# Kernel tuning notes

Hardware: AMD Instinct MI355X
Metric: run time of the kernel (lower is better)

## Reference

```python
import jax, jax.numpy as jnp
import numpy as np

C = 128          # hidden_channels
N = 100000       # num nodes
E = 500000       # num edges
BN_EPS = 1e-5    # BatchNorm eps (training mode: batch statistics)


def _bn_relu(x, g, b):
    # BatchNorm1d (training mode, biased variance) followed by ReLU
    mu = x.mean(axis=0)
    var = x.var(axis=0)
    return jax.nn.relu(g * (x - mu) * jax.lax.rsqrt(var + BN_EPS) + b)


def setup_inputs() -> dict:
    key = jax.random.key(0)
    ks = jax.random.split(key, 10)
    f = lambda k, s: jax.random.normal(k, s, dtype=jnp.float32) * 0.05
    return {
        "node_rep": f(ks[0], (N, C)),
        "edge_rep": f(ks[1], (E, C)),
        "endpoints": jax.random.randint(ks[2], (2, E), 0, N, dtype=jnp.int64)
            if jax.config.jax_enable_x64 else jax.random.randint(ks[2], (2, E), 0, N, dtype=jnp.int32),
        # lvl_mlp_1: Linear(2C -> C, no bias) + BN(C)
        "W_lvl1": f(ks[3], (2 * C, C)),
        "g_lvl1": jnp.ones((C,), jnp.float32), "b_lvl1": jnp.zeros((C,), jnp.float32),
        # lvl_mlp_2: Linear(C->2C) + BN(2C) + ReLU + Linear(2C->C) + BN(C) + ReLU
        "W_n1": f(ks[4], (C, 2 * C)),
        "g_n1": jnp.ones((2 * C,), jnp.float32), "b_n1": jnp.zeros((2 * C,), jnp.float32),
        "W_n2": f(ks[5], (2 * C, C)),
        "g_n2": jnp.ones((C,), jnp.float32), "b_n2": jnp.zeros((C,), jnp.float32),
        # lift_mlp: Linear(C->2C) + BN(2C) + ReLU + Linear(2C->C) + BN(C) + ReLU
        "W_e1": f(ks[6], (C, 2 * C)),
        "g_e1": jnp.ones((2 * C,), jnp.float32), "b_e1": jnp.zeros((2 * C,), jnp.float32),
        "W_e2": f(ks[7], (2 * C, C)),
        "g_e2": jnp.ones((C,), jnp.float32), "b_e2": jnp.zeros((C,), jnp.float32),
        "eps1": jnp.zeros((), jnp.float32),
        "eps2": jnp.zeros((), jnp.float32),
    }


def reference(node_rep, edge_rep, endpoints,
              W_lvl1, g_lvl1, b_lvl1,
              W_n1, g_n1, b_n1, W_n2, g_n2, b_n2,
              W_e1, g_e1, b_e1, W_e2, g_e2, b_e2,
              eps1, eps2):
    s, t = endpoints[0], endpoints[1]
    # transfer0_0 node->edge: each edge sums its two endpoint node features
    lift_aggr = node_rep[s] + node_rep[t]                       # [E, C]
    h = _bn_relu(jnp.concatenate([lift_aggr, edge_rep], -1) @ W_lvl1,
                 g_lvl1, b_lvl1)                                # [E, C]
    # reverse transfer edge->node: scatter-add to both endpoints
    lvl_aggr = jnp.zeros_like(node_rep).at[s].add(h).at[t].add(h)  # [N, C]
    node_in = (1.0 + eps1) * node_rep + lvl_aggr
    node_out = _bn_relu(_bn_relu(node_in @ W_n1, g_n1, b_n1) @ W_n2, g_n2, b_n2)
    edge_in = (1.0 + eps2) * edge_rep + lift_aggr
    edge_out = _bn_relu(_bn_relu(edge_in @ W_e1, g_e1, b_e1) @ W_e2, g_e2, b_e2)
    return (node_out, edge_out)
```

## Files before the change

kernel.cpp:

```cpp
#include <hip/hip_runtime.h>

#define NN 100000
#define NE 500000

typedef short v8s __attribute__((ext_vector_type(8)));
typedef float v4f __attribute__((ext_vector_type(4)));

__device__ __forceinline__ unsigned short f2bf(float f) {
    unsigned u = __float_as_uint(f);
    u += 0x7fffu + ((u >> 16) & 1u);
    return (unsigned short)(u >> 16);
}
__device__ __forceinline__ float bf2f(unsigned short h) {
    return __uint_as_float(((unsigned)h) << 16);
}
__device__ __forceinline__ unsigned pk2(float a, float b) {
    return (unsigned)f2bf(a) | ((unsigned)f2bf(b) << 16);
}
__device__ __forceinline__ float lo16(unsigned v) { return bf2f((unsigned short)(v & 0xffffu)); }
__device__ __forceinline__ float hi16(unsigned v) { return bf2f((unsigned short)(v >> 16)); }

__global__ void detect_k(const unsigned short* __restrict__ edgeR, int* __restrict__ flag) {
    __shared__ int cnt;
    const int tid = threadIdx.x;
    if (tid == 0) cnt = 0;
    __syncthreads();
    const float v = fabsf(bf2f(edgeR[2 * tid]));
    const int sane = (v > 1e-5f && v < 100.f) ? 1 : 0;
    atomicAdd(&cnt, sane);
    __syncthreads();
    if (tid == 0) *flag = (cnt >= 128) ? 1 : 0;
}

__global__ __launch_bounds__(256) void convert_k(const void* __restrict__ src,
    unsigned short* __restrict__ dst, const long n4, const int* __restrict__ flag)
{
    const long i = (long)blockIdx.x * 256 + threadIdx.x;
    if (i >= n4) return;
    if (*flag) {
        ((uint2*)dst)[i] = ((const uint2*)src)[i];
    } else {
        const float4 f = ((const float4*)src)[i];
        uint2 o; o.x = pk2(f.x, f.y); o.y = pk2(f.z, f.w);
        ((uint2*)dst)[i] = o;
    }
}

__global__ __launch_bounds__(256) void pack_weights(
    const void* __restrict__ W1, const void* __restrict__ Wn1,
    const void* __restrict__ Wn2, const void* __restrict__ We1,
    const void* __restrict__ We2, unsigned short* __restrict__ wpk,
    const int* __restrict__ flag)
{
    const int i = blockIdx.x * 256 + threadIdx.x;
    if (i >= 163840) return;
    const void* W; int Nn; int li = i;
    if (i < 32768)       { W = W1;  Nn = 128; }
    else if (i < 65536)  { W = Wn1; Nn = 256; li -= 32768; }
    else if (i < 98304)  { W = Wn2; Nn = 128; li -= 65536; }
    else if (i < 131072) { W = We1; Nn = 256; li -= 98304; }
    else                 { W = We2; Nn = 128; li -= 131072; }
    const int ntn = Nn >> 4;
    const int j = li & 7, l = (li >> 3) & 63, tile = li >> 9;
    const int ct = tile % ntn, kt = tile / ntn;
    const int k = kt * 32 + (l >> 4) * 8 + j;
    const int n = ct * 16 + (l & 15);
    const int idx = k * Nn + n;
    wpk[i] = (*flag) ? ((const unsigned short*)W)[idx]
                     : f2bf(((const float*)W)[idx]);
}

__global__ __launch_bounds__(256) void kernel_A(
    const unsigned short* __restrict__ node, const unsigned short* __restrict__ edge,
    const int* __restrict__ ep,
    const unsigned short* __restrict__ wpk1, const unsigned short* __restrict__ wpkE1,
    unsigned short* __restrict__ y1, unsigned short* __restrict__ w1,
    float* __restrict__ stats, const void* __restrict__ eps2p, const int* __restrict__ flag)
{
    __shared__ unsigned short X[64][264];
    const int tid = threadIdx.x, wid = tid >> 6, lane = tid & 63;
    const int mrow = lane & 15, quad = lane >> 4;
    const long e0 = (long)blockIdx.x * 64;
    const int bin = blockIdx.x & 7;

    for (int rr = 0; rr < 16; ++rr) {
        const int r = wid * 16 + rr;
        const long e = e0 + r;
        unsigned lp = 0, epk = 0;
        if (e < NE) {
            const int s = ep[e], t = ep[NE + e];
            const unsigned a = ((const unsigned*)(node + (size_t)s * 128))[lane];
            const unsigned b = ((const unsigned*)(node + (size_t)t * 128))[lane];
            epk = ((const unsigned*)(edge + (size_t)e * 128))[lane];
            lp = pk2(lo16(a) + lo16(b), hi16(a) + hi16(b));
        }
        *(unsigned*)&X[r][2 * lane] = lp;
        *(unsigned*)&X[r][128 + 2 * lane] = epk;
    }
    __syncthreads();

    {
        v4f acc[4][2];
        #pragma unroll
        for (int rb = 0; rb < 4; ++rb)
            #pragma unroll
            for (int c = 0; c < 2; ++c)
                acc[rb][c] = (v4f){0.f, 0.f, 0.f, 0.f};
        const int ct0 = wid * 2;
        #pragma unroll
        for (int kt = 0; kt < 8; ++kt) {
            v8s a[4];
            #pragma unroll
            for (int rb = 0; rb < 4; ++rb)
                a[rb] = *(const v8s*)&X[rb * 16 + mrow][kt * 32 + quad * 8];
            #pragma unroll
            for (int c = 0; c < 2; ++c) {
                const v8s b = ((const v8s*)wpk1)[(kt * 8 + ct0 + c) * 64 + lane];
                #pragma unroll
                for (int rb = 0; rb < 4; ++rb)
                    acc[rb][c] = __builtin_amdgcn_mfma_f32_16x16x32_bf16(a[rb], b, acc[rb][c], 0, 0, 0);
            }
        }
        #pragma unroll
        for (int c = 0; c < 2; ++c) {
            const int col = (ct0 + c) * 16 + mrow;
            float sy = 0.f, sq = 0.f;
            #pragma unroll
            for (int rb = 0; rb < 4; ++rb) {
                #pragma unroll
                for (int r4 = 0; r4 < 4; ++r4) {
                    const float v = acc[rb][c][r4];
                    const long e = e0 + rb * 16 + quad * 4 + r4;
                    if (e < NE) y1[e * 128 + col] = f2bf(v);
                    sy += v; sq += v * v;
                }
            }
            sy += __shfl_xor(sy, 16); sy += __shfl_xor(sy, 32);
            sq += __shfl_xor(sq, 16); sq += __shfl_xor(sq, 32);
            if (quad == 0) {
                atomicAdd(&stats[bin * 1792 + col], sy);
                atomicAdd(&stats[bin * 1792 + 128 + col], sq);
            }
        }
    }
    __syncthreads();

    const float e2 = 1.f + ((*flag) ? bf2f(((const unsigned short*)eps2p)[0])
                                    : ((const float*)eps2p)[0]);
    for (int rr = 0; rr < 16; ++rr) {
        const int r = wid * 16 + rr;
        const unsigned lp = *(const unsigned*)&X[r][2 * lane];
        const unsigned ee = *(const unsigned*)&X[r][128 + 2 * lane];
        *(unsigned*)&X[r][2 * lane] = pk2(fmaf(e2, lo16(ee), lo16(lp)),
                                          fmaf(e2, hi16(ee), hi16(lp)));
    }
    __syncthreads();

    {
        v4f acc[4][4];
        #pragma unroll
        for (int rb = 0; rb < 4; ++rb)
            #pragma unroll
            for (int c = 0; c < 4; ++c)
                acc[rb][c] = (v4f){0.f, 0.f, 0.f, 0.f};
        const int ct0 = wid * 4;
        #pragma unroll
        for (int kt = 0; kt < 4; ++kt) {
            v8s a[4];
            #pragma unroll
            for (int rb = 0; rb < 4; ++rb)
                a[rb] = *(const v8s*)&X[rb * 16 + mrow][kt * 32 + quad * 8];
            #pragma unroll
            for (int c = 0; c < 4; ++c) {
                const v8s b = ((const v8s*)wpkE1)[(kt * 16 + ct0 + c) * 64 + lane];
                #pragma unroll
                for (int rb = 0; rb < 4; ++rb)
                    acc[rb][c] = __builtin_amdgcn_mfma_f32_16x16x32_bf16(a[rb], b, acc[rb][c], 0, 0, 0);
            }
        }
        #pragma unroll
        for (int c = 0; c < 4; ++c) {
            const int col = (ct0 + c) * 16 + mrow;
            float sy = 0.f, sq = 0.f;
            #pragma unroll
            for (int rb = 0; rb < 4; ++rb) {
                #pragma unroll
                for (int r4 = 0; r4 < 4; ++r4) {
                    const float v = acc[rb][c][r4];
                    const long e = e0 + rb * 16 + quad * 4 + r4;
                    if (e < NE) w1[e * 256 + col] = f2bf(v);
                    sy += v; sq += v * v;
                }
            }
            sy += __shfl_xor(sy, 16); sy += __shfl_xor(sy, 32);
            sq += __shfl_xor(sq, 16); sq += __shfl_xor(sq, 32);
            if (quad == 0) {
                atomicAdd(&stats[bin * 1792 + 256 + col], sy);
                atomicAdd(&stats[bin * 1792 + 512 + col], sq);
            }
        }
    }
}

__global__ void finalize_k(const float* __restrict__ stats, float* __restrict__ ab,
                           const void* __restrict__ g, const void* __restrict__ bb,
                           const int sOff, const int qOff, const int aOff, const int bOff,
                           const int n, const float invc, const int* __restrict__ flag)
{
    const int c = threadIdx.x;
    if (c >= n) return;
    float S = 0.f, Q = 0.f;
    for (int b = 0; b < 8; ++b) { S += stats[b * 1792 + sOff + c]; Q += stats[b * 1792 + qOff + c]; }
    const float mu = S * invc;
    const float var = Q * invc - mu * mu;
    const float gv = (*flag) ? bf2f(((const unsigned short*)g)[c]) : ((const float*)g)[c];
    const float bv = (*flag) ? bf2f(((const unsigned short*)bb)[c]) : ((const float*)bb)[c];
    const float a = gv * rsqrtf(var + 1e-5f);
    ab[aOff + c] = a;
    ab[bOff + c] = bv - a * mu;
}

__global__ __launch_bounds__(256) void scatter_k(
    const unsigned short* __restrict__ y1, const int* __restrict__ ep,
    const float* __restrict__ ab, float* __restrict__ acc)
{
    const int gw = (blockIdx.x * 256 + threadIdx.x) >> 6;
    const int lane = threadIdx.x & 63;
    const int nw = (gridDim.x * 256) >> 6;
    const int c0 = 2 * lane;
    const float a0 = ab[c0], a1 = ab[c0 + 1];
    const float b0 = ab[128 + c0], b1 = ab[128 + c0 + 1];
    for (long e = gw; e < NE; e += nw) {
        const unsigned v = *(const unsigned*)(y1 + e * 128 + c0);
        const float h0 = fmaxf(fmaf(a0, lo16(v), b0), 0.f);
        const float h1 = fmaxf(fmaf(a1, hi16(v), b1), 0.f);
        const int s = ep[e], t = ep[NE + e];
        atomicAdd(&acc[(size_t)s * 128 + c0], h0);
        atomicAdd(&acc[(size_t)s * 128 + c0 + 1], h1);
        atomicAdd(&acc[(size_t)t * 128 + c0], h0);
        atomicAdd(&acc[(size_t)t * 128 + c0 + 1], h1);
    }
}

__global__ __launch_bounds__(256) void gemm_node1(
    const unsigned short* __restrict__ node, const float* __restrict__ aggr,
    const unsigned short* __restrict__ wpk, unsigned short* __restrict__ z1,
    float* __restrict__ sS, float* __restrict__ sQ,
    const void* __restrict__ eps1p, const int* __restrict__ flag)
{
    __shared__ unsigned short X[64][136];
    const int tid = threadIdx.x, wid = tid >> 6, lane = tid & 63;
    const int mrow = lane & 15, quad = lane >> 4;
    const long r0 = (long)blockIdx.x * 64;
    const int bin = blockIdx.x & 7;
    const float ea = 1.f + ((*flag) ? bf2f(((const unsigned short*)eps1p)[0])
                                    : ((const float*)eps1p)[0]);
    for (int rr = 0; rr < 16; ++rr) {
        const int r = wid * 16 + rr;
        const long gr = r0 + r;
        unsigned o = 0;
        if (gr < NN) {
            const unsigned nr = ((const unsigned*)(node + (size_t)gr * 128))[lane];
            const float2 ag = ((const float2*)(aggr + (size_t)gr * 128))[lane];
            o = pk2(fmaf(ea, lo16(nr), ag.x), fmaf(ea, hi16(nr), ag.y));
        }
        *(unsigned*)&X[r][2 * lane] = o;
    }
    __syncthreads();
    v4f acc[4][4];
    #pragma unroll
    for (int rb = 0; rb < 4; ++rb)
        #pragma unroll
        for (int c = 0; c < 4; ++c)
            acc[rb][c] = (v4f){0.f, 0.f, 0.f, 0.f};
    const int ct0 = wid * 4;
    #pragma unroll
    for (int kt = 0; kt < 4; ++kt) {
        v8s a[4];
        #pragma unroll
        for (int rb = 0; rb < 4; ++rb)
            a[rb] = *(const v8s*)&X[rb * 16 + mrow][kt * 32 + quad * 8];
        #pragma unroll
        for (int c = 0; c < 4; ++c) {
            const v8s b = ((const v8s*)wpk)[(kt * 16 + ct0 + c) * 64 + lane];
            #pragma unroll
            for (int rb = 0; rb < 4; ++rb)
                acc[rb][c] = __builtin_amdgcn_mfma_f32_16x16x32_bf16(a[rb], b, acc[rb][c], 0, 0, 0);
        }
    }
    #pragma unroll
    for (int c = 0; c < 4; ++c) {
        const int col = (ct0 + c) * 16 + mrow;
        float sy = 0.f, sq = 0.f;
        #pragma unroll
        for (int rb = 0; rb < 4; ++rb) {
            #pragma unroll
            for (int r4 = 0; r4 < 4; ++r4) {
                const float v = acc[rb][c][r4];
                const long gr = r0 + rb * 16 + quad * 4 + r4;
                if (gr < NN) z1[gr * 256 + col] = f2bf(v);
                sy += v; sq += v * v;
            }
        }
        sy += __shfl_xor(sy, 16); sy += __shfl_xor(sy, 32);
        sq += __shfl_xor(sq, 16); sq += __shfl_xor(sq, 32);
        if (quad == 0) {
            atomicAdd(&sS[bin * 1792 + col], sy);
            atomicAdd(&sQ[bin * 1792 + col], sq);
        }
    }
}

__global__ __launch_bounds__(256) void gemm_k256(
    const unsigned short* __restrict__ in, const float* __restrict__ aab,
    const float* __restrict__ bab, const unsigned short* __restrict__ wpk,
    unsigned short* __restrict__ out, float* __restrict__ sS, float* __restrict__ sQ,
    const long rows)
{
    __shared__ unsigned short X[64][264];
    const int tid = threadIdx.x, wid = tid >> 6, lane = tid & 63;
    const int mrow = lane & 15, quad = lane >> 4;
    const long r0 = (long)blockIdx.x * 64;
    const int bin = blockIdx.x & 7;
    const float4 av = ((const float4*)aab)[lane];
    const float4 bv = ((const float4*)bab)[lane];
    for (int rr = 0; rr < 16; ++rr) {
        const int r = wid * 16 + rr;
        const long gr = r0 + r;
        ushort4 o = {0, 0, 0, 0};
        if (gr < rows) {
            const ushort4 w = *(const ushort4*)(in + gr * 256 + 4 * lane);
            o.x = f2bf(fmaxf(fmaf(av.x, bf2f(w.x), bv.x), 0.f));
            o.y = f2bf(fmaxf(fmaf(av.y, bf2f(w.y), bv.y), 0.f));
            o.z = f2bf(fmaxf(fmaf(av.z, bf2f(w.z), bv.z), 0.f));
            o.w = f2bf(fmaxf(fmaf(av.w, bf2f(w.w), bv.w), 0.f));
        }
        *(ushort4*)&X[r][4 * lane] = o;
    }
    __syncthreads();
    v4f acc[4][2];
    #pragma unroll
    for (int rb = 0; rb < 4; ++rb)
        #pragma unroll
        for (int c = 0; c < 2; ++c)
            acc[rb][c] = (v4f){0.f, 0.f, 0.f, 0.f};
    const int ct0 = wid * 2;
    #pragma unroll
    for (int kt = 0; kt < 8; ++kt) {
        v8s a[4];
        #pragma unroll
        for (int rb = 0; rb < 4; ++rb)
            a[rb] = *(const v8s*)&X[rb * 16 + mrow][kt * 32 + quad * 8];
        #pragma unroll
        for (int c = 0; c < 2; ++c) {
            const v8s b = ((const v8s*)wpk)[(kt * 8 + ct0 + c) * 64 + lane];
            #pragma unroll
            for (int rb = 0; rb < 4; ++rb)
                acc[rb][c] = __builtin_amdgcn_mfma_f32_16x16x32_bf16(a[rb], b, acc[rb][c], 0, 0, 0);
        }
    }
    #pragma unroll
    for (int c = 0; c < 2; ++c) {
        const int col = (ct0 + c) * 16 + mrow;
        float sy = 0.f, sq = 0.f;
        #pragma unroll
        for (int rb = 0; rb < 4; ++rb) {
            #pragma unroll
            for (int r4 = 0; r4 < 4; ++r4) {
                const float v = acc[rb][c][r4];
                const long gr = r0 + rb * 16 + quad * 4 + r4;
                if (gr < rows) out[gr * 128 + col] = f2bf(v);
                sy += v; sq += v * v;
            }
        }
        sy += __shfl_xor(sy, 16); sy += __shfl_xor(sy, 32);
        sq += __shfl_xor(sq, 16); sq += __shfl_xor(sq, 32);
        if (quad == 0) {
            atomicAdd(&sS[bin * 1792 + col], sy);
            atomicAdd(&sQ[bin * 1792 + col], sq);
        }
    }
}

__global__ __launch_bounds__(256) void final_k(
    const unsigned short* __restrict__ z2, const unsigned short* __restrict__ w2,
    const float* __restrict__ ab, void* __restrict__ out, const int* __restrict__ flag)
{
    const long p = (long)blockIdx.x * 256 + threadIdx.x;
    const long npn = (long)NN * 64;
    const long tot = npn + (long)NE * 64;
    if (p >= tot) return;
    long el, oe; const unsigned short* src; int abA, abB;
    if (p < npn) { el = p * 2; oe = el; src = z2; abA = 1536; abB = 1664; }
    else { el = (p - npn) * 2; oe = (long)NN * 128 + el; src = w2; abA = 1280; abB = 1408; }
    const int col = (int)(el & 127);
    const unsigned v = *(const unsigned*)(src + el);
    const float o0 = fmaxf(fmaf(ab[abA + col], lo16(v), ab[abB + col]), 0.f);
    const float o1 = fmaxf(fmaf(ab[abA + col + 1], hi16(v), ab[abB + col + 1]), 0.f);
    if (*flag) {
        *(unsigned*)((unsigned short*)out + oe) = pk2(o0, o1);
    } else {
        float2 f; f.x = o0; f.y = o1;
        *(float2*)((float*)out + oe) = f;
    }
}

extern "C" void kernel_launch(void* const* d_in, const int* in_sizes, int n_in,
                              void* d_out, int out_size, void* d_ws, size_t ws_size,
                              hipStream_t stream)
{
    (void)in_sizes; (void)n_in; (void)out_size; (void)ws_size;
    const unsigned short* edgeR = (const unsigned short*)d_in[1];
    const int* ep = (const int*)d_in[2];

    char* ws = (char*)d_ws;
    unsigned short* wpk = (unsigned short*)ws;
    float* stats = (float*)(ws + 327680);
    float* ab    = (float*)(ws + 385024);
    int* flag    = (int*)(ws + 392192);
    float* acc   = (float*)(ws + 392448);
    unsigned short* nodeC = (unsigned short*)(ws + 51592448);
    unsigned short* edgeC = (unsigned short*)(ws + 77192448);
    unsigned short* y1    = (unsigned short*)(ws + 205192448);
    unsigned short* w1    = (unsigned short*)(ws + 333192448);
    unsigned short* w2 = edgeC;
    unsigned short* z1 = y1;
    unsigned short* z2 = y1 + 25600000;

    const unsigned short* wpk1  = wpk;
    const unsigned short* wpkN1 = wpk + 32768;
    const unsigned short* wpkN2 = wpk + 65536;
    const unsigned short* wpkE1 = wpk + 98304;
    const unsigned short* wpkE2 = wpk + 131072;

    detect_k<<<1, 256, 0, stream>>>(edgeR, flag);
    hipMemsetAsync(stats, 0, 57344, stream);
    hipMemsetAsync(acc, 0, (size_t)NN * 128 * 4, stream);
    convert_k<<<12500, 256, 0, stream>>>(d_in[0], nodeC, 3200000, flag);
    convert_k<<<62500, 256, 0, stream>>>(d_in[1], edgeC, 16000000, flag);
    pack_weights<<<640, 256, 0, stream>>>(d_in[3], d_in[6], d_in[9], d_in[12], d_in[15], wpk, flag);

    kernel_A<<<7813, 256, 0, stream>>>(nodeC, edgeC, ep, wpk1, wpkE1, y1, w1, stats, d_in[19], flag);
    finalize_k<<<1, 128, 0, stream>>>(stats, ab, d_in[4], d_in[5], 0, 128, 0, 128, 128, 1.f / NE, flag);
    finalize_k<<<1, 256, 0, stream>>>(stats, ab, d_in[13], d_in[14], 256, 512, 256, 512, 256, 1.f / NE, flag);

    scatter_k<<<2048, 256, 0, stream>>>(y1, ep, ab, acc);

    gemm_k256<<<7813, 256, 0, stream>>>(w1, ab + 256, ab + 512, wpkE2, w2, stats + 1280, stats + 1408, (long)NE);
    finalize_k<<<1, 128, 0, stream>>>(stats, ab, d_in[16], d_in[17], 1280, 1408, 1280, 1408, 128, 1.f / NE, flag);

    gemm_node1<<<1563, 256, 0, stream>>>(nodeC, acc, wpkN1, z1, stats + 768, stats + 1024, d_in[18], flag);
    finalize_k<<<1, 256, 0, stream>>>(stats, ab, d_in[7], d_in[8], 768, 1024, 768, 1024, 256, 1.f / NN, flag);

    gemm_k256<<<1563, 256, 0, stream>>>(z1, ab + 768, ab + 1024, wpkN2, z2, stats + 1536, stats + 1664, (long)NN);
    finalize_k<<<1, 128, 0, stream>>>(stats, ab, d_in[10], d_in[11], 1536, 1664, 1536, 1664, 128, 1.f / NN, flag);

    final_k<<<150000, 256, 0, stream>>>(z2, w2, ab, d_out, flag);
}
```

Before: 2.093 ms.

## Replace atomic scatter with CSR gather and drop input conversion passes

```diff
diff --git a/kernel.cpp b/kernel.cpp
--- a/kernel.cpp
+++ b/kernel.cpp
@@ -20,6 +20,12 @@
 __device__ __forceinline__ float lo16(unsigned v) { return bf2f((unsigned short)(v & 0xffffu)); }
 __device__ __forceinline__ float hi16(unsigned v) { return bf2f((unsigned short)(v >> 16)); }
 
+__device__ __forceinline__ unsigned load2(const void* base, long row, int lane, int f) {
+    if (f) return ((const unsigned*)base)[row * 64 + lane];
+    const float2 v = ((const float2*)base)[row * 64 + lane];
+    return pk2(v.x, v.y);
+}
+
 __global__ void detect_k(const unsigned short* __restrict__ edgeR, int* __restrict__ flag) {
     __shared__ int cnt;
     const int tid = threadIdx.x;
@@ -32,18 +38,48 @@
     if (tid == 0) *flag = (cnt >= 128) ? 1 : 0;
 }
 
-__global__ __launch_bounds__(256) void convert_k(const void* __restrict__ src,
-    unsigned short* __restrict__ dst, const long n4, const int* __restrict__ flag)
-{
-    const long i = (long)blockIdx.x * 256 + threadIdx.x;
-    if (i >= n4) return;
-    if (*flag) {
-        ((uint2*)dst)[i] = ((const uint2*)src)[i];
-    } else {
-        const float4 f = ((const float4*)src)[i];
-        uint2 o; o.x = pk2(f.x, f.y); o.y = pk2(f.z, f.w);
-        ((uint2*)dst)[i] = o;
-    }
+__global__ __launch_bounds__(256) void hist_k(const int* __restrict__ ep, int* __restrict__ deg) {
+    const int i = blockIdx.x * 256 + threadIdx.x;
+    if (i < 2 * NE) atomicAdd(&deg[ep[i]], 1);
+}
+
+__global__ __launch_bounds__(1024) void scan_k(int* __restrict__ degcur, int* __restrict__ rowptr) {
+    __shared__ int sd[1024];
+    const int t = threadIdx.x;
+    const int base = t * 98;
+    int sum = 0;
+    for (int i = 0; i < 98; ++i) {
+        const int idx = base + i;
+        if (idx < NN) sum += degcur[idx];
+    }
+    sd[t] = sum;
+    __syncthreads();
+    for (int off = 1; off < 1024; off <<= 1) {
+        const int v = (t >= off) ? sd[t - off] : 0;
+        __syncthreads();
+        sd[t] += v;
+        __syncthreads();
+    }
+    int run = sd[t] - sum;
+    for (int i = 0; i < 98; ++i) {
+        const int idx = base + i;
+        if (idx < NN) {
+            const int d = degcur[idx];
+            rowptr[idx] = run;
+            degcur[idx] = run;
+            run += d;
+        }
+    }
+    if (t == 0) rowptr[NN] = 2 * NE;
+}
+
+__global__ __launch_bounds__(256) void fill_k(const int* __restrict__ ep,
+                                              int* __restrict__ cursor, int* __restrict__ csr) {
+    const int i = blockIdx.x * 256 + threadIdx.x;
+    if (i >= 2 * NE) return;
+    const int n = ep[i];
+    const int pos = atomicAdd(&cursor[n], 1);
+    csr[pos] = (i < NE) ? i : (i - NE);
 }
 
 __global__ __launch_bounds__(256) void pack_weights(
@@ -71,7 +107,7 @@
 }
 
 __global__ __launch_bounds__(256) void kernel_A(
-    const unsigned short* __restrict__ node, const unsigned short* __restrict__ edge,
+    const void* __restrict__ node, const void* __restrict__ edge,
     const int* __restrict__ ep,
     const unsigned short* __restrict__ wpk1, const unsigned short* __restrict__ wpkE1,
     unsigned short* __restrict__ y1, unsigned short* __restrict__ w1,
@@ -82,6 +118,7 @@
     const int mrow = lane & 15, quad = lane >> 4;
     const long e0 = (long)blockIdx.x * 64;
     const int bin = blockIdx.x & 7;
+    const int f = *flag;
 
     for (int rr = 0; rr < 16; ++rr) {
         const int r = wid * 16 + rr;
@@ -89,9 +126,9 @@
         unsigned lp = 0, epk = 0;
         if (e < NE) {
             const int s = ep[e], t = ep[NE + e];
-            const unsigned a = ((const unsigned*)(node + (size_t)s * 128))[lane];
-            const unsigned b = ((const unsigned*)(node + (size_t)t * 128))[lane];
-            epk = ((const unsigned*)(edge + (size_t)e * 128))[lane];
+            const unsigned a = load2(node, s, lane, f);
+            const unsigned b = load2(node, t, lane, f);
+            epk = load2(edge, e, lane, f);
             lp = pk2(lo16(a) + lo16(b), hi16(a) + hi16(b));
         }
         *(unsigned*)&X[r][2 * lane] = lp;
@@ -145,8 +182,8 @@
     }
     __syncthreads();
 
-    const float e2 = 1.f + ((*flag) ? bf2f(((const unsigned short*)eps2p)[0])
-                                    : ((const float*)eps2p)[0]);
+    const float e2 = 1.f + (f ? bf2f(((const unsigned short*)eps2p)[0])
+                              : ((const float*)eps2p)[0]);
     for (int rr = 0; rr < 16; ++rr) {
         const int r = wid * 16 + rr;
         const unsigned lp = *(const unsigned*)&X[r][2 * lane];
@@ -220,53 +257,46 @@
     ab[bOff + c] = bv - a * mu;
 }
 
-__global__ __launch_bounds__(256) void scatter_k(
-    const unsigned short* __restrict__ y1, const int* __restrict__ ep,
-    const float* __restrict__ ab, float* __restrict__ acc)
-{
-    const int gw = (blockIdx.x * 256 + threadIdx.x) >> 6;
-    const int lane = threadIdx.x & 63;
-    const int nw = (gridDim.x * 256) >> 6;
-    const int c0 = 2 * lane;
-    const float a0 = ab[c0], a1 = ab[c0 + 1];
-    const float b0 = ab[128 + c0], b1 = ab[128 + c0 + 1];
-    for (long e = gw; e < NE; e += nw) {
-        const unsigned v = *(const unsigned*)(y1 + e * 128 + c0);
-        const float h0 = fmaxf(fmaf(a0, lo16(v), b0), 0.f);
-        const float h1 = fmaxf(fmaf(a1, hi16(v), b1), 0.f);
-        const int s = ep[e], t = ep[NE + e];
-        atomicAdd(&acc[(size_t)s * 128 + c0], h0);
-        atomicAdd(&acc[(size_t)s * 128 + c0 + 1], h1);
-        atomicAdd(&acc[(size_t)t * 128 + c0], h0);
-        atomicAdd(&acc[(size_t)t * 128 + c0 + 1], h1);
-    }
-}
-
 __global__ __launch_bounds__(256) void gemm_node1(
-    const unsigned short* __restrict__ node, const float* __restrict__ aggr,
+    const void* __restrict__ node, const unsigned short* __restrict__ y1,
+    const int* __restrict__ rowptr, const int* __restrict__ csr,
     const unsigned short* __restrict__ wpk, unsigned short* __restrict__ z1,
     float* __restrict__ sS, float* __restrict__ sQ,
-    const void* __restrict__ eps1p, const int* __restrict__ flag)
+    const void* __restrict__ eps1p, const float* __restrict__ ab,
+    const int* __restrict__ flag)
 {
     __shared__ unsigned short X[64][136];
     const int tid = threadIdx.x, wid = tid >> 6, lane = tid & 63;
     const int mrow = lane & 15, quad = lane >> 4;
     const long r0 = (long)blockIdx.x * 64;
     const int bin = blockIdx.x & 7;
-    const float ea = 1.f + ((*flag) ? bf2f(((const unsigned short*)eps1p)[0])
-                                    : ((const float*)eps1p)[0]);
+    const int f = *flag;
+    const float ea = 1.f + (f ? bf2f(((const unsigned short*)eps1p)[0])
+                              : ((const float*)eps1p)[0]);
+    const int c0 = 2 * lane;
+    const float a0 = ab[c0], a1 = ab[c0 + 1];
+    const float b0 = ab[128 + c0], b1 = ab[128 + c0 + 1];
+
     for (int rr = 0; rr < 16; ++rr) {
         const int r = wid * 16 + rr;
         const long gr = r0 + r;
         unsigned o = 0;
         if (gr < NN) {
-            const unsigned nr = ((const unsigned*)(node + (size_t)gr * 128))[lane];
-            const float2 ag = ((const float2*)(aggr + (size_t)gr * 128))[lane];
-            o = pk2(fmaf(ea, lo16(nr), ag.x), fmaf(ea, hi16(nr), ag.y));
+            float s0 = 0.f, s1 = 0.f;
+            const int beg = rowptr[gr], end = rowptr[gr + 1];
+            for (int i = beg; i < end; ++i) {
+                const int e = csr[i];
+                const unsigned v = ((const unsigned*)y1)[(size_t)e * 64 + lane];
+                s0 += fmaxf(fmaf(a0, lo16(v), b0), 0.f);
+                s1 += fmaxf(fmaf(a1, hi16(v), b1), 0.f);
+            }
+            const unsigned nr = load2(node, gr, lane, f);
+            o = pk2(fmaf(ea, lo16(nr), s0), fmaf(ea, hi16(nr), s1));
         }
         *(unsigned*)&X[r][2 * lane] = o;
     }
     __syncthreads();
+
     v4f acc[4][4];
     #pragma unroll
     for (int rb = 0; rb < 4; ++rb)
@@ -415,17 +445,17 @@
 
     char* ws = (char*)d_ws;
     unsigned short* wpk = (unsigned short*)ws;
-    float* stats = (float*)(ws + 327680);
-    float* ab    = (float*)(ws + 385024);
-    int* flag    = (int*)(ws + 392192);
-    float* acc   = (float*)(ws + 392448);
-    unsigned short* nodeC = (unsigned short*)(ws + 51592448);
-    unsigned short* edgeC = (unsigned short*)(ws + 77192448);
-    unsigned short* y1    = (unsigned short*)(ws + 205192448);
-    unsigned short* w1    = (unsigned short*)(ws + 333192448);
-    unsigned short* w2 = edgeC;
-    unsigned short* z1 = y1;
-    unsigned short* z2 = y1 + 25600000;
+    float* stats   = (float*)(ws + 327680);
+    float* ab      = (float*)(ws + 385024);
+    int*   flag    = (int*)(ws + 392192);
+    int*   rowptr  = (int*)(ws + 392448);
+    int*   cursor  = (int*)(ws + 792576);
+    int*   csr     = (int*)(ws + 1192704);
+    unsigned short* y1 = (unsigned short*)(ws + 5192704);
+    unsigned short* w1 = (unsigned short*)(ws + 133192704);
+    unsigned short* w2 = (unsigned short*)(ws + 389192704);
+    unsigned short* z1 = (unsigned short*)(ws + 517192704);
+    unsigned short* z2 = (unsigned short*)(ws + 568392704);
 
     const unsigned short* wpk1  = wpk;
     const unsigned short* wpkN1 = wpk + 32768;
@@ -435,25 +465,29 @@
 
     detect_k<<<1, 256, 0, stream>>>(edgeR, flag);
     hipMemsetAsync(stats, 0, 57344, stream);
-    hipMemsetAsync(acc, 0, (size_t)NN * 128 * 4, stream);
-    convert_k<<<12500, 256, 0, stream>>>(d_in[0], nodeC, 3200000, flag);
-    convert_k<<<62500, 256, 0, stream>>>(d_in[1], edgeC, 16000000, flag);
+    hipMemsetAsync(cursor, 0, 400000, stream);
+
+    hist_k<<<3907, 256, 0, stream>>>(ep, cursor);
+    scan_k<<<1, 1024, 0, stream>>>(cursor, rowptr);
+    fill_k<<<3907, 256, 0, stream>>>(ep, cursor, csr);
+
     pack_weights<<<640, 256, 0, stream>>>(d_in[3], d_in[6], d_in[9], d_in[12], d_in[15], wpk, flag);
 
-    kernel_A<<<7813, 256, 0, stream>>>(nodeC, edgeC, ep, wpk1, wpkE1, y1, w1, stats, d_in[19], flag);
+    kernel_A<<<7813, 256, 0, stream>>>(d_in[0], d_in[1], ep, wpk1, wpkE1, y1, w1, stats, d_in[19], flag);
     finalize_k<<<1, 128, 0, stream>>>(stats, ab, d_in[4], d_in[5], 0, 128, 0, 128, 128, 1.f / NE, flag);
     finalize_k<<<1, 256, 0, stream>>>(stats, ab, d_in[13], d_in[14], 256, 512, 256, 512, 256, 1.f / NE, flag);
 
-    scatter_k<<<2048, 256, 0, stream>>>(y1, ep, ab, acc);
-
-    gemm_k256<<<7813, 256, 0, stream>>>(w1, ab + 256, ab + 512, wpkE2, w2, stats + 1280, stats + 1408, (long)NE);
+    gemm_node1<<<1563, 256, 0, stream>>>(d_in[0], y1, rowptr, csr, wpkN1, z1,
+                                         stats + 768, stats + 1024, d_in[18], ab, flag);
+    finalize_k<<<1, 256, 0, stream>>>(stats, ab, d_in[7], d_in[8], 768, 1024, 768, 1024, 256, 1.f / NN, flag);
+
+    gemm_k256<<<1563, 256, 0, stream>>>(z1, ab + 768, ab + 1024, wpkN2, z2,
+                                        stats + 1536, stats + 1664, (long)NN);
+    finalize_k<<<1, 128, 0, stream>>>(stats, ab, d_in[10], d_in[11], 1536, 1664, 1536, 1664, 128, 1.f / NN, flag);
+
+    gemm_k256<<<7813, 256, 0, stream>>>(w1, ab + 256, ab + 512, wpkE2, w2,
+                                        stats + 1280, stats + 1408, (long)NE);
     finalize_k<<<1, 128, 0, stream>>>(stats, ab, d_in[16], d_in[17], 1280, 1408, 1280, 1408, 128, 1.f / NE, flag);
 
-    gemm_node1<<<1563, 256, 0, stream>>>(nodeC, acc, wpkN1, z1, stats + 768, stats + 1024, d_in[18], flag);
-    finalize_k<<<1, 256, 0, stream>>>(stats, ab, d_in[7], d_in[8], 768, 1024, 768, 1024, 256, 1.f / NN, flag);
-
-    gemm_k256<<<1563, 256, 0, stream>>>(z1, ab + 768, ab + 1024, wpkN2, z2, stats + 1536, stats + 1664, (long)NN);
-    finalize_k<<<1, 128, 0, stream>>>(stats, ab, d_in[10], d_in[11], 1536, 1664, 1536, 1664, 128, 1.f / NN, flag);
-
     final_k<<<150000, 256, 0, stream>>>(z2, w2, ab, d_out, flag);
 }
```

After: 2.050 ms. -2.1%, faster.
